# Performance work log

Measured on AMD Instinct MI355X. Metric: run time of the kernel, lower is better.

The kernel has to match this reference:

```python
import jax, jax.numpy as jnp
import numpy as np

B, N, C, H, M, T, L = 2, 4096, 256, 8, 48, 10000, 256
CH = C // H
HID = 512  # mlp_ratio=2


def _ln(x, g, b, eps=1e-5):
    mu = x.mean(-1, keepdims=True)
    var = ((x - mu) ** 2).mean(-1, keepdims=True)
    return (x - mu) * jax.lax.rsqrt(var + eps) * g + b


def setup_inputs() -> dict:
    key = jax.random.key(0)
    ks = iter(jax.random.split(key, 40))
    nrm = lambda shape, s=0.02: jax.random.normal(next(ks), shape, jnp.float32) * s
    return dict(
        feat=jax.random.normal(next(ks), (B, N, C), jnp.float32),
        memory=jax.random.normal(next(ks), (B, L, C), jnp.float32),
        member_idx=jax.random.randint(next(ks), (B, N, M), 0, N),
        cluster_mask=jax.random.randint(next(ks), (B, N, M), 0, 2, jnp.int32),
        pe_idx=jax.random.randint(next(ks), (B, N, M), 0, T),
        global_attn=0,
        pre_table=jax.random.normal(next(ks), (T, 5), jnp.float32),
        Wq=nrm((C, C)), bq=jnp.zeros(C), Wkv=nrm((C, 2 * C)), bkv=jnp.zeros(2 * C),
        blank_k=nrm((C,), 1.0), blank_v=nrm((C,), 1.0),
        Wpe=nrm((5, H)), bpe=jnp.zeros(H),
        Wproj=nrm((C, C)), bproj=jnp.zeros(C),
        g1=jnp.ones(C), be1=jnp.zeros(C), g2=jnp.ones(C), be2=jnp.zeros(C),
        xWq=nrm((C, C)), xbq=jnp.zeros(C), xWk=nrm((C, C)), xbk=jnp.zeros(C),
        xWv=nrm((C, C)), xbv=jnp.zeros(C), xWo=nrm((C, C)), xbo=jnp.zeros(C),
        xg=jnp.ones(C), xbe=jnp.zeros(C),
        W1=nrm((C, HID)), bf1=jnp.zeros(HID), W2=nrm((HID, C)), bf2=jnp.zeros(C),
    )


def _cluster_attn(x, member_idx, cluster_mask, pe_idx, pre_table,
                  Wq, bq, Wkv, bkv, blank_k, blank_v, Wpe, bpe, Wproj, bproj):
    b, n, c = x.shape
    scale = CH ** -0.5
    q = ((x @ Wq + bq) * scale).reshape(b, n, H, CH).transpose(0, 2, 1, 3)  # bhnc
    kv = (x @ Wkv + bkv).reshape(b, n, H, 2, CH)
    k = kv[..., 0, :].transpose(0, 2, 1, 3)  # bhnc
    v = kv[..., 1, :].transpose(0, 2, 1, 3)  # bhnc
    # CLUSTENQK: gather per-token neighborhood keys, dot with q -> b h n m
    gather = jax.vmap(lambda t, idx: t[:, idx, :])  # (h,n,c),(n,m)->(h,n,m,c)
    k_g = gather(k, member_idx)
    attn = jnp.einsum('bhnc,bhnmc->bhnm', q, k_g)
    # positional embedding table lookup
    pe_table = pre_table @ Wpe + bpe                 # T x H
    pos = pe_table[pe_idx].transpose(0, 3, 1, 2)     # b h n m
    attn = attn + pos
    maskf = cluster_mask.astype(attn.dtype)[:, None]  # b 1 n m
    attn = attn + (1.0 - maskf) * -100.0
    blank_attn = jnp.einsum('bhnc,hc->bhn', q, blank_k.reshape(H, CH))[..., None]
    p = jax.nn.softmax(jnp.concatenate([attn, blank_attn], axis=-1), axis=-1)
    pa, pb = p[..., :-1], p[..., -1:]
    # CLUSTENAV: gather values, weighted sum
    v_g = gather(v, member_idx)
    out = jnp.einsum('bhnm,bhnmc->bhnc', pa, v_g)
    out = out + pb * blank_v.reshape(1, H, 1, CH)
    out = out.transpose(0, 2, 1, 3).reshape(b, n, c)
    return out @ Wproj + bproj


def _cross_attn(tgt, memory, xWq, xbq, xWk, xbk, xWv, xbv, xWo, xbo, xg, xbe):
    b, n, c = tgt.shape
    t2 = _ln(tgt, xg, xbe)  # normalize_before=True
    q = (t2 @ xWq + xbq).reshape(b, n, H, CH).transpose(0, 2, 1, 3) * (CH ** -0.5)
    k = (memory @ xWk + xbk).reshape(b, -1, H, CH).transpose(0, 2, 1, 3)
    v = (memory @ xWv + xbv).reshape(b, -1, H, CH).transpose(0, 2, 1, 3)
    p = jax.nn.softmax(jnp.einsum('bhnc,bhlc->bhnl', q, k), axis=-1)
    o = jnp.einsum('bhnl,bhlc->bhnc', p, v).transpose(0, 2, 1, 3).reshape(b, n, c)
    return tgt + (o @ xWo + xbo)


def reference(feat, memory, member_idx, cluster_mask, pe_idx, global_attn, pre_table,
              Wq, bq, Wkv, bkv, blank_k, blank_v, Wpe, bpe, Wproj, bproj,
              g1, be1, g2, be2,
              xWq, xbq, xWk, xbk, xWv, xbv, xWo, xbo, xg, xbe,
              W1, bf1, W2, bf2):
    # global_attn is a static flag; this reference covers the local-cluster path
    assert global_attn == 0
    # local cluster attention with pre-norm residual (drop_path/layer_scale disabled)
    feat = feat + _cluster_attn(_ln(feat, g1, be1), member_idx, cluster_mask, pe_idx,
                                pre_table, Wq, bq, Wkv, bkv, blank_k, blank_v,
                                Wpe, bpe, Wproj, bproj)
    # cross attention to memory (pre-norm, residual inside)
    feat = _cross_attn(feat, memory, xWq, xbq, xWk, xbk, xWv, xbv, xWo, xbo, xg, xbe)
    # MLP block
    h = jax.nn.gelu(_ln(feat, g2, be2) @ W1 + bf1, approximate=False)
    feat = feat + (h @ W2 + bf2)
    return feat
```

## Files before the change

kernel.cpp:

```cpp
#include <hip/hip_runtime.h>
#include <hip/hip_bf16.h>
#include <hip/hip_fp8.h>
#include <math.h>

#define BB 2
#define NN 4096
#define CC 256
#define HH 8
#define MM 48
#define TT 10000
#define LL 256
#define CHDIM 32
#define HIDD 512
#define ROWS (BB*NN)

typedef __attribute__((ext_vector_type(8))) short bf16x8;
typedef __attribute__((ext_vector_type(4))) float f32x4;
typedef __attribute__((ext_vector_type(2))) float f32x2;

static __device__ __forceinline__ short f2bf(float x) {
    __hip_bfloat16 h = __float2bfloat16(x);
    return *reinterpret_cast<short*>(&h);
}
static __device__ __forceinline__ float bf2f(short s) {
    unsigned int u = ((unsigned int)(unsigned short)s) << 16;
    union { unsigned int u; float f; } c; c.u = u;
    return c.f;
}

struct WtDesc { const float* src; __hip_bfloat16* dst; int K; int N; int tile0; float scl; };
struct WtArgs { WtDesc d[9]; };

__global__ __launch_bounds__(256) void prep_all_kernel(WtArgs a,
    const float* __restrict__ pre, const float* __restrict__ Wpe,
    const float* __restrict__ bpe, float* __restrict__ pet,
    const float* __restrict__ bq, const float* __restrict__ bkv,
    const float* __restrict__ xbk, const float* __restrict__ xbv,
    const float* __restrict__ xbq, float scale,
    float* __restrict__ bqkv, float* __restrict__ xbkv, float* __restrict__ xbqS,
    const float* __restrict__ memory, __hip_bfloat16* __restrict__ memBf) {
    __shared__ float tile[32][33];
    int bid = blockIdx.x, tid = threadIdx.x;
    if (bid < 768) {
        int mi = 0;
        #pragma unroll
        for (int i = 1; i < 9; ++i) if (bid >= a.d[i].tile0) mi = i;
        WtDesc dsc = a.d[mi];
        int t = bid - dsc.tile0;
        int tiles_n = dsc.N >> 5;
        int k0 = (t / tiles_n) * 32, n0 = (t % tiles_n) * 32;
        int tx = tid & 31, ty = tid >> 5;
        #pragma unroll
        for (int i = 0; i < 32; i += 8)
            tile[ty + i][tx] = dsc.src[(size_t)(k0 + ty + i) * dsc.N + n0 + tx];
        __syncthreads();
        #pragma unroll
        for (int i = 0; i < 32; i += 8)
            dsc.dst[(size_t)(n0 + ty + i) * dsc.K + k0 + tx] = __float2bfloat16(tile[tx][ty + i] * dsc.scl);
        return;
    }
    bid -= 768;
    if (bid < 313) {
        int i = bid * 256 + tid;
        if (i >= TT * HH) return;
        int t = i / HH, h = i % HH;
        float s = bpe[h];
        #pragma unroll
        for (int j = 0; j < 5; ++j) s += pre[t * 5 + j] * Wpe[j * HH + h];
        pet[i] = s;
    } else if (bid < 319) {
        int i = (bid - 313) * 256 + tid;
        if (i < 256) bqkv[i] = bq[i] * scale;
        else if (i < 768) bqkv[i] = bkv[i - 256];
        else if (i < 1024) xbkv[i - 768] = xbk[i - 768];
        else if (i < 1280) xbkv[256 + i - 1024] = xbv[i - 1024];
        else if (i < 1536) xbqS[i - 1280] = xbq[i - 1280] * scale;
    } else {
        int i = (bid - 319) * 256 + tid;
        if (i < 131072) memBf[i] = __float2bfloat16(memory[i]);
    }
}

__global__ __launch_bounds__(256) void ln_kernel(const float* __restrict__ in,
                                                 const float* __restrict__ g,
                                                 const float* __restrict__ b,
                                                 __hip_bfloat16* __restrict__ out) {
    int wave = threadIdx.x >> 6, lane = threadIdx.x & 63;
    int row = blockIdx.x * 4 + wave;
    float4 v = ((const float4*)(in + (size_t)row * CC))[lane];
    float s = (v.x + v.y) + (v.z + v.w);
    #pragma unroll
    for (int off = 32; off; off >>= 1) s += __shfl_xor(s, off, 64);
    float mu = s * (1.0f / 256.0f);
    float dx = v.x - mu, dy = v.y - mu, dz = v.z - mu, dw = v.w - mu;
    float s2 = (dx * dx + dy * dy) + (dz * dz + dw * dw);
    #pragma unroll
    for (int off = 32; off; off >>= 1) s2 += __shfl_xor(s2, off, 64);
    float rs = rsqrtf(s2 * (1.0f / 256.0f) + 1e-5f);
    float4 g4 = ((const float4*)g)[lane];
    float4 b4 = ((const float4*)b)[lane];
    ushort4 o4;
    o4.x = (unsigned short)f2bf(dx * rs * g4.x + b4.x);
    o4.y = (unsigned short)f2bf(dy * rs * g4.y + b4.y);
    o4.z = (unsigned short)f2bf(dz * rs * g4.z + b4.z);
    o4.w = (unsigned short)f2bf(dw * rs * g4.w + b4.w);
    *(ushort4*)((unsigned short*)out + (size_t)row * CC + lane * 4) = o4;
}

#define GBM 64
#define GBN 64
#define GBK 64
#define LDA 72
template<int ACT, int OUTM>
__device__ __forceinline__ void gemm_body(short* As, short* Bs,
    const __hip_bfloat16* __restrict__ A, const __hip_bfloat16* __restrict__ BT,
    const float* __restrict__ bias, void* __restrict__ outv,
    const float* __restrict__ residual, int N, int K, int row0, int col0,
    void* __restrict__ outv2) {
    int tid = threadIdx.x;
    int lane = tid & 63, wid = tid >> 6;
    int wr = wid >> 1, wc = wid & 1;
    int lr = lane & 15, lk = lane >> 4;
    f32x4 acc[2][2] = {};
    for (int kt = 0; kt < K; kt += GBK) {
        #pragma unroll
        for (int i = 0; i < 2; ++i) {
            int flat = tid + i * 256;
            int r = flat >> 3, kc = (flat & 7) * 8;
            *(bf16x8*)&As[r * LDA + kc] = *(const bf16x8*)(A + (size_t)(row0 + r) * K + kt + kc);
        }
        #pragma unroll
        for (int i = 0; i < 2; ++i) {
            int flat = tid + i * 256;
            int r = flat >> 3, kc = (flat & 7) * 8;
            *(bf16x8*)&Bs[r * LDA + kc] = *(const bf16x8*)(BT + (size_t)(col0 + r) * K + kt + kc);
        }
        __syncthreads();
        #pragma unroll
        for (int ks = 0; ks < 2; ++ks) {
            bf16x8 bfr[2];
            #pragma unroll
            for (int n = 0; n < 2; ++n)
                bfr[n] = *(const bf16x8*)&Bs[(wc * 32 + n * 16 + lr) * LDA + ks * 32 + lk * 8];
            #pragma unroll
            for (int m = 0; m < 2; ++m) {
                bf16x8 afr = *(const bf16x8*)&As[(wr * 32 + m * 16 + lr) * LDA + ks * 32 + lk * 8];
                #pragma unroll
                for (int n = 0; n < 2; ++n)
                    acc[m][n] = __builtin_amdgcn_mfma_f32_16x16x32_bf16(afr, bfr[n], acc[m][n], 0, 0, 0);
            }
        }
        __syncthreads();
    }
    float bv[2];
    #pragma unroll
    for (int n = 0; n < 2; ++n) bv[n] = bias[col0 + wc * 32 + n * 16 + lr];
    #pragma unroll
    for (int m = 0; m < 2; ++m) {
        #pragma unroll
        for (int n = 0; n < 2; ++n) {
            int col = col0 + wc * 32 + n * 16 + lr;
            #pragma unroll
            for (int r = 0; r < 4; ++r) {
                int row = row0 + wr * 32 + m * 16 + lk * 4 + r;
                float v = acc[m][n][r] + bv[n];
                if (ACT == 1) {
                    float z = v + 0.044715f * v * v * v;
                    v = v / (1.0f + __expf(-1.5957691216057308f * z));
                }
                if (OUTM == 2) {
                    if (col < 256) {
                        ((__hip_bfloat16*)outv)[(size_t)row * 256 + col] = __float2bfloat16(v);
                    } else {
                        __hip_fp8_e4m3 f8(v);
                        ((unsigned char*)outv2)[(size_t)row * 512 + (col - 256)] = f8.__x;
                    }
                } else {
                    size_t oi = (size_t)row * N + col;
                    if (residual) v += residual[oi];
                    if (OUTM == 1) ((__hip_bfloat16*)outv)[oi] = __float2bfloat16(v);
                    else ((float*)outv)[oi] = v;
                }
            }
        }
    }
}

template<int ACT, int OUTM>
__global__ __launch_bounds__(256) void mfma_gemm_kernel(
    const __hip_bfloat16* __restrict__ A, const __hip_bfloat16* __restrict__ BT,
    const float* __restrict__ bias, void* __restrict__ outv,
    const float* __restrict__ residual, int M, int N, int K,
    void* __restrict__ outv2) {
    __shared__ short As[GBM * LDA];
    __shared__ short Bs[GBN * LDA];
    gemm_body<ACT, OUTM>(As, Bs, A, BT, bias, outv, residual, N, K,
                         blockIdx.y * GBM, blockIdx.x * GBN, outv2);
}

struct GemmPair {
    const __hip_bfloat16 *A1, *B1; const float* bias1; void* out1;
    const __hip_bfloat16 *A2, *B2; const float* bias2; void* out2;
};
__global__ __launch_bounds__(256) void dual_gemm_kernel(GemmPair p) {
    __shared__ short As[GBM * LDA];
    __shared__ short Bs[GBN * LDA];
    if (blockIdx.x < 4) {
        gemm_body<0, 1>(As, Bs, p.A1, p.B1, p.bias1, p.out1, nullptr, 256, 256,
                        blockIdx.y * GBM, blockIdx.x * GBN, nullptr);
    } else {
        int row0 = blockIdx.y * GBM;
        if (row0 >= 512) return;
        gemm_body<0, 1>(As, Bs, p.A2, p.B2, p.bias2, p.out2, nullptr, 512, 256,
                        row0, (blockIdx.x - 4) * GBN, nullptr);
    }
}

#define KVSTR8 528
__global__ __launch_bounds__(512) void cluster_attn_kernel(
    const __hip_bfloat16* __restrict__ qh,
    const unsigned char* __restrict__ kv8,
    const int* __restrict__ member_idx, const int* __restrict__ cluster_mask,
    const int* __restrict__ pe_idx, const float* __restrict__ pet,
    const float* __restrict__ blank_k, const float* __restrict__ blank_v,
    __hip_bfloat16* __restrict__ outp) {
    const short* qg = (const short*)qh;
    __shared__ unsigned char s_kv[48 * KVSTR8];
    __shared__ float s_pm[48 * 9];
    __shared__ float s_q[256];
    int tid = threadIdx.x;
    int bid = blockIdx.x;
    int row = ((bid & 7) << 10) | (bid >> 3);
    int b = row >> 12;

    {
        int w = tid >> 6, l = tid & 63;
        #pragma unroll
        for (int r = 0; r < 6; ++r) {
            int m = w + r * 8;
            int im = member_idx[(size_t)row * MM + m];
            uint2 v8 = *(const uint2*)(kv8 + ((size_t)(b * NN + im)) * 512 + l * 8);
            *(uint2*)&s_kv[m * KVSTR8 + l * 8] = v8;
        }
    }
    if (tid < MM) {
        float mb = cluster_mask[(size_t)row * MM + tid] ? 0.0f : -100.0f;
        int pidx = pe_idx[(size_t)row * MM + tid];
        const float4* pr = (const float4*)(pet + (size_t)pidx * 8);
        float4 p0 = pr[0], p1 = pr[1];
        float* dst = &s_pm[tid * 9];
        dst[0] = p0.x + mb; dst[1] = p0.y + mb; dst[2] = p0.z + mb; dst[3] = p0.w + mb;
        dst[4] = p1.x + mb; dst[5] = p1.y + mb; dst[6] = p1.z + mb; dst[7] = p1.w + mb;
    } else if (tid >= 256) {
        s_q[tid - 256] = bf2f(qg[(size_t)row * CC + (tid - 256)]);
    }
    __syncthreads();

    int h = tid >> 6, lane = tid & 63;
    const float* qf = s_q + h * CHDIM;
    float e = 0.0f;
    if (lane < MM) {
        const uint4* kp = (const uint4*)(s_kv + lane * KVSTR8 + h * 64);
        uint4 kw0 = kp[0];
        uint4 kw1 = kp[1];
        unsigned int kws[8] = {kw0.x, kw0.y, kw0.z, kw0.w, kw1.x, kw1.y, kw1.z, kw1.w};
        float d0 = s_pm[lane * 9 + h], d1 = 0.0f;
        #pragma unroll
        for (int u = 0; u < 8; u += 2) {
            f32x2 a01 = __builtin_amdgcn_cvt_pk_f32_fp8(kws[u], 0);
            f32x2 a23 = __builtin_amdgcn_cvt_pk_f32_fp8(kws[u], 1);
            f32x2 b01 = __builtin_amdgcn_cvt_pk_f32_fp8(kws[u + 1], 0);
            f32x2 b23 = __builtin_amdgcn_cvt_pk_f32_fp8(kws[u + 1], 1);
            d0 += qf[u * 4 + 0] * a01.x + qf[u * 4 + 1] * a01.y
                + qf[u * 4 + 2] * a23.x + qf[u * 4 + 3] * a23.y;
            d1 += qf[u * 4 + 4] * b01.x + qf[u * 4 + 5] * b01.y
                + qf[u * 4 + 6] * b23.x + qf[u * 4 + 7] * b23.y;
        }
        e = __expf(d0 + d1);
    } else if (lane == MM) {
        const float* bk = blank_k + h * CHDIM;
        float d = 0.0f;
        #pragma unroll
        for (int c = 0; c < CHDIM; ++c) d += qf[c] * bk[c];
        e = __expf(d);
    }
    float ssum = e;
    #pragma unroll
    for (int off = 32; off; off >>= 1) ssum += __shfl_xor(ssum, off, 64);
    float p = e / ssum;
    float p48 = __shfl(p, MM, 64);

    int mg = lane >> 3, cq = lane & 7;
    unsigned int vw[6];
    #pragma unroll
    for (int it = 0; it < 6; ++it)
        vw[it] = *(const unsigned int*)(s_kv + (it * 8 + mg) * KVSTR8 + h * 64 + 32 + cq * 4);
    float a0 = 0.f, a1 = 0.f, a2 = 0.f, a3 = 0.f;
    #pragma unroll
    for (int it = 0; it < 6; ++it) {
        int m = it * 8 + mg;
        float pm = __shfl(p, m, 64);
        f32x2 v01 = __builtin_amdgcn_cvt_pk_f32_fp8(vw[it], 0);
        f32x2 v23 = __builtin_amdgcn_cvt_pk_f32_fp8(vw[it], 1);
        a0 += pm * v01.x; a1 += pm * v01.y;
        a2 += pm * v23.x; a3 += pm * v23.y;
    }
    #pragma unroll
    for (int off = 8; off < 64; off <<= 1) {
        a0 += __shfl_xor(a0, off, 64);
        a1 += __shfl_xor(a1, off, 64);
        a2 += __shfl_xor(a2, off, 64);
        a3 += __shfl_xor(a3, off, 64);
    }
    if (lane < 8) {
        const float* bvp = blank_v + h * CHDIM + cq * 4;
        a0 += p48 * bvp[0]; a1 += p48 * bvp[1]; a2 += p48 * bvp[2]; a3 += p48 * bvp[3];
        ushort4 o4;
        o4.x = (unsigned short)f2bf(a0); o4.y = (unsigned short)f2bf(a1);
        o4.z = (unsigned short)f2bf(a2); o4.w = (unsigned short)f2bf(a3);
        *(ushort4*)((unsigned short*)outp + (size_t)row * CC + h * CHDIM + cq * 4) = o4;
    }
}

#define KSLD 40
#define PVLD 264
__global__ __launch_bounds__(256) void cross_attn_kernel(
    const __hip_bfloat16* __restrict__ xq,
    const __hip_bfloat16* __restrict__ xkvh,
    __hip_bfloat16* __restrict__ o) {
    const short* xkv = (const short*)xkvh;
    extern __shared__ short lds[];
    short* Ks = lds;
    short* Vt = lds + 256 * KSLD;
    short* Ps = Vt + 32 * PVLD;
    int tid = threadIdx.x, lane = tid & 63, w = tid >> 6;
    int tile = blockIdx.x, h = blockIdx.y, b = blockIdx.z;
    int lr = lane & 15, g = lane >> 4;

    #pragma unroll
    for (int p = 0; p < 8; ++p) {
        int l = p * 32 + (tid >> 3);
        int c4 = (tid & 7) * 4;
        const short* kvrow = xkv + ((size_t)(b * LL + l)) * 512 + h * CHDIM;
        ushort4 kk = *(const ushort4*)(kvrow + c4);
        *(ushort4*)&Ks[l * KSLD + c4] = kk;
        ushort4 vv = *(const ushort4*)(kvrow + 256 + c4);
        Vt[(c4 + 0) * PVLD + l] = vv.x;
        Vt[(c4 + 1) * PVLD + l] = vv.y;
        Vt[(c4 + 2) * PVLD + l] = vv.z;
        Vt[(c4 + 3) * PVLD + l] = vv.w;
    }
    __syncthreads();

    int qrow = b * NN + tile * 64 + w * 16 + lr;
    bf16x8 afr = *(const bf16x8*)(xq + (size_t)qrow * CC + h * CHDIM + g * 8);
    f32x4 s[16];
    #pragma unroll
    for (int t = 0; t < 16; ++t) {
        bf16x8 kb = *(const bf16x8*)&Ks[(t * 16 + lr) * KSLD + g * 8];
        s[t] = __builtin_amdgcn_mfma_f32_16x16x32_bf16(afr, kb, (f32x4){0.f,0.f,0.f,0.f}, 0, 0, 0);
    }
    float rs[4] = {0.f, 0.f, 0.f, 0.f};
    #pragma unroll
    for (int t = 0; t < 16; ++t)
        #pragma unroll
        for (int r = 0; r < 4; ++r) { float e = __expf(s[t][r]); s[t][r] = e; rs[r] += e; }
    #pragma unroll
    for (int off = 1; off < 16; off <<= 1)
        #pragma unroll
        for (int r = 0; r < 4; ++r) rs[r] += __shfl_xor(rs[r], off, 64);
    short* Pw = Ps + w * 16 * PVLD;
    #pragma unroll
    for (int t = 0; t < 16; ++t)
        #pragma unroll
        for (int r = 0; r < 4; ++r)
            Pw[(g * 4 + r) * PVLD + t * 16 + lr] = f2bf(s[t][r]);
    f32x4 oacc[2] = {};
    #pragma unroll
    for (int kc = 0; kc < 8; ++kc) {
        bf16x8 pa = *(const bf16x8*)&Pw[lr * PVLD + kc * 32 + g * 8];
        #pragma unroll
        for (int n = 0; n < 2; ++n) {
            bf16x8 vb = *(const bf16x8*)&Vt[(n * 16 + lr) * PVLD + kc * 32 + g * 8];
            oacc[n] = __builtin_amdgcn_mfma_f32_16x16x32_bf16(pa, vb, oacc[n], 0, 0, 0);
        }
    }
    float inv[4];
    #pragma unroll
    for (int r = 0; r < 4; ++r) inv[r] = 1.0f / rs[r];
    #pragma unroll
    for (int n = 0; n < 2; ++n)
        #pragma unroll
        for (int r = 0; r < 4; ++r) {
            int orow = b * NN + tile * 64 + w * 16 + g * 4 + r;
            o[(size_t)orow * CC + h * CHDIM + n * 16 + lr] = __float2bfloat16(oacc[n][r] * inv[r]);
        }
}

extern "C" void kernel_launch(void* const* d_in, const int* in_sizes, int n_in,
                              void* d_out, int out_size, void* d_ws, size_t ws_size,
                              hipStream_t stream) {
    const float* feat        = (const float*)d_in[0];
    const float* memory      = (const float*)d_in[1];
    const int*   member_idx  = (const int*)d_in[2];
    const int*   cluster_mask= (const int*)d_in[3];
    const int*   pe_idx      = (const int*)d_in[4];
    const float* pre_table   = (const float*)d_in[6];
    const float* Wq    = (const float*)d_in[7];
    const float* bq    = (const float*)d_in[8];
    const float* Wkv   = (const float*)d_in[9];
    const float* bkv   = (const float*)d_in[10];
    const float* blank_k = (const float*)d_in[11];
    const float* blank_v = (const float*)d_in[12];
    const float* Wpe   = (const float*)d_in[13];
    const float* bpe   = (const float*)d_in[14];
    const float* Wproj = (const float*)d_in[15];
    const float* bproj = (const float*)d_in[16];
    const float* g1    = (const float*)d_in[17];
    const float* be1   = (const float*)d_in[18];
    const float* g2    = (const float*)d_in[19];
    const float* be2   = (const float*)d_in[20];
    const float* xWq   = (const float*)d_in[21];
    const float* xbq   = (const float*)d_in[22];
    const float* xWk   = (const float*)d_in[23];
    const float* xbk   = (const float*)d_in[24];
    const float* xWv   = (const float*)d_in[25];
    const float* xbv   = (const float*)d_in[26];
    const float* xWo   = (const float*)d_in[27];
    const float* xbo   = (const float*)d_in[28];
    const float* xg    = (const float*)d_in[29];
    const float* xbe   = (const float*)d_in[30];
    const float* W1    = (const float*)d_in[31];
    const float* bf1   = (const float*)d_in[32];
    const float* W2    = (const float*)d_in[33];
    const float* bf2   = (const float*)d_in[34];
    float* out = (float*)d_out;
    float* ws  = (float*)d_ws;

    __hip_bfloat16* qBf   = (__hip_bfloat16*)ws;
    __hip_bfloat16* xqBf  = (__hip_bfloat16*)ws;
    unsigned char*  kv8   = (unsigned char*)(ws + 1048576);
    __hip_bfloat16* xkvBf = (__hip_bfloat16*)(ws + 2097152);
    __hip_bfloat16* hBf   = (__hip_bfloat16*)(ws + 2228224);
    float* feat1F = ws + 4325376;
    __hip_bfloat16* aBf   = (__hip_bfloat16*)(ws + 6422528);
    __hip_bfloat16* oBf   = (__hip_bfloat16*)(ws + 7471104);
    __hip_bfloat16* WqkvT = (__hip_bfloat16*)(ws + 8519680);
    __hip_bfloat16* WprojT= (__hip_bfloat16*)(ws + 8617984);
    __hip_bfloat16* xWqT  = (__hip_bfloat16*)(ws + 8650752);
    __hip_bfloat16* xWoT  = (__hip_bfloat16*)(ws + 8683520);
    __hip_bfloat16* xWkvT = (__hip_bfloat16*)(ws + 8716288);
    __hip_bfloat16* W1T   = (__hip_bfloat16*)(ws + 8781824);
    __hip_bfloat16* W2T   = (__hip_bfloat16*)(ws + 8847360);
    __hip_bfloat16* memBf = (__hip_bfloat16*)(ws + 8912896);
    float* pet   = ws + 8978432;
    float* bqkv  = ws + 9058432;
    float* xbkv  = ws + 9059200;
    float* xbqS  = ws + 9059712;

    const float scale = 0.17677669529663689f;

    WtArgs wa;
    wa.d[0] = { Wq,    WqkvT,          256, 256, 0,   scale };
    wa.d[1] = { Wkv,   WqkvT + 65536,  256, 512, 64,  1.0f };
    wa.d[2] = { Wproj, WprojT,         256, 256, 192, 1.0f };
    wa.d[3] = { xWq,   xWqT,           256, 256, 256, scale };
    wa.d[4] = { xWk,   xWkvT,          256, 256, 320, 1.0f };
    wa.d[5] = { xWv,   xWkvT + 65536,  256, 256, 384, 1.0f };
    wa.d[6] = { xWo,   xWoT,           256, 256, 448, 1.0f };
    wa.d[7] = { W1,    W1T,            256, 512, 512, 1.0f };
    wa.d[8] = { W2,    W2T,            512, 256, 640, 1.0f };
    prep_all_kernel<<<768 + 831, 256, 0, stream>>>(wa, pre_table, Wpe, bpe, pet,
                                                   bq, bkv, xbk, xbv, xbq, scale,
                                                   bqkv, xbkv, xbqS, memory, memBf);

    ln_kernel<<<ROWS / 4, 256, 0, stream>>>(feat, g1, be1, aBf);
    mfma_gemm_kernel<0,2><<<dim3(12, 128), 256, 0, stream>>>(aBf, WqkvT, bqkv, qBf, nullptr, ROWS, 768, 256, kv8);
    cluster_attn_kernel<<<ROWS, 512, 0, stream>>>(qBf, kv8, member_idx, cluster_mask, pe_idx, pet, blank_k, blank_v, oBf);
    mfma_gemm_kernel<0,0><<<dim3(4, 128), 256, 0, stream>>>(oBf, WprojT, bproj, feat1F, feat, ROWS, 256, 256, nullptr);
    ln_kernel<<<ROWS / 4, 256, 0, stream>>>(feat1F, xg, xbe, aBf);
    {
        GemmPair gp;
        gp.A1 = aBf;   gp.B1 = xWqT;  gp.bias1 = xbqS; gp.out1 = xqBf;
        gp.A2 = memBf; gp.B2 = xWkvT; gp.bias2 = xbkv; gp.out2 = xkvBf;
        dual_gemm_kernel<<<dim3(12, 128), 256, 0, stream>>>(gp);
    }
    {
        size_t xlds = (256 * KSLD + 32 * PVLD + 4 * 16 * PVLD) * sizeof(short);
        cross_attn_kernel<<<dim3(NN / 64, HH, BB), 256, xlds, stream>>>(xqBf, xkvBf, oBf);
    }
    mfma_gemm_kernel<0,0><<<dim3(4, 128), 256, 0, stream>>>(oBf, xWoT, xbo, out, feat1F, ROWS, 256, 256, nullptr);
    ln_kernel<<<ROWS / 4, 256, 0, stream>>>(out, g2, be2, aBf);
    mfma_gemm_kernel<1,1><<<dim3(8, 128), 256, 0, stream>>>(aBf, W1T, bf1, hBf, nullptr, ROWS, HIDD, 256, nullptr);
    mfma_gemm_kernel<0,0><<<dim3(4, 128), 256, 0, stream>>>(hBf, W2T, bf2, out, out, ROWS, 256, HIDD, nullptr);
}
```

Measured before the change: 148.8 us.

## Process two rows per cluster-attention block with prefetched second-row gather

Each cluster attention block now handles two consecutive rows. The second row's KV gather and q load are issued into registers before the first row's compute runs, so they overlap with it, and are then staged into a second LDS buffer. The PE/mask bias is now read directly per lane from global memory instead of being staged in LDS, and the LDS row stride is reduced. This halves the block count and hides gather latency, at the cost of extra registers, an extra barrier and less parallelism per block.

```diff
diff --git a/kernel.cpp b/kernel.cpp
--- a/kernel.cpp
+++ b/kernel.cpp
@@ -216,7 +216,78 @@
     }
 }
 
-#define KVSTR8 528
+#define KVSTR8 520
+__device__ __forceinline__ void cluster_compute_row(
+    const unsigned char* s_kvr, const float* s_qr, int row, int b, int w, int lane,
+    const int* __restrict__ cluster_mask, const int* __restrict__ pe_idx,
+    const float* __restrict__ pet, const float* __restrict__ blank_k,
+    const float* __restrict__ blank_v, __hip_bfloat16* __restrict__ outp) {
+    int h = w;
+    const float* qf = s_qr + h * CHDIM;
+    float e = 0.0f;
+    if (lane < MM) {
+        const unsigned int* kp = (const unsigned int*)(s_kvr + lane * KVSTR8 + h * 64);
+        float d0 = pet[(size_t)pe_idx[(size_t)row * MM + lane] * HH + h];
+        if (cluster_mask[(size_t)row * MM + lane] == 0) d0 -= 100.0f;
+        float d1 = 0.0f;
+        #pragma unroll
+        for (int u = 0; u < 8; u += 2) {
+            unsigned int ka = kp[u], kb = kp[u + 1];
+            f32x2 a01 = __builtin_amdgcn_cvt_pk_f32_fp8(ka, 0);
+            f32x2 a23 = __builtin_amdgcn_cvt_pk_f32_fp8(ka, 1);
+            f32x2 b01 = __builtin_amdgcn_cvt_pk_f32_fp8(kb, 0);
+            f32x2 b23 = __builtin_amdgcn_cvt_pk_f32_fp8(kb, 1);
+            d0 += qf[u * 4 + 0] * a01.x + qf[u * 4 + 1] * a01.y
+                + qf[u * 4 + 2] * a23.x + qf[u * 4 + 3] * a23.y;
+            d1 += qf[u * 4 + 4] * b01.x + qf[u * 4 + 5] * b01.y
+                + qf[u * 4 + 6] * b23.x + qf[u * 4 + 7] * b23.y;
+        }
+        e = __expf(d0 + d1);
+    } else if (lane == MM) {
+        const float* bk = blank_k + h * CHDIM;
+        float d = 0.0f;
+        #pragma unroll
+        for (int c = 0; c < CHDIM; ++c) d += qf[c] * bk[c];
+        e = __expf(d);
+    }
+    float ssum = e;
+    #pragma unroll
+    for (int off = 32; off; off >>= 1) ssum += __shfl_xor(ssum, off, 64);
+    float p = e / ssum;
+    float p48 = __shfl(p, MM, 64);
+
+    int mg = lane >> 3, cq = lane & 7;
+    unsigned int vw[6];
+    #pragma unroll
+    for (int it = 0; it < 6; ++it)
+        vw[it] = *(const unsigned int*)(s_kvr + (it * 8 + mg) * KVSTR8 + h * 64 + 32 + cq * 4);
+    float a0 = 0.f, a1 = 0.f, a2 = 0.f, a3 = 0.f;
+    #pragma unroll
+    for (int it = 0; it < 6; ++it) {
+        int m = it * 8 + mg;
+        float pm = __shfl(p, m, 64);
+        f32x2 v01 = __builtin_amdgcn_cvt_pk_f32_fp8(vw[it], 0);
+        f32x2 v23 = __builtin_amdgcn_cvt_pk_f32_fp8(vw[it], 1);
+        a0 += pm * v01.x; a1 += pm * v01.y;
+        a2 += pm * v23.x; a3 += pm * v23.y;
+    }
+    #pragma unroll
+    for (int off = 8; off < 64; off <<= 1) {
+        a0 += __shfl_xor(a0, off, 64);
+        a1 += __shfl_xor(a1, off, 64);
+        a2 += __shfl_xor(a2, off, 64);
+        a3 += __shfl_xor(a3, off, 64);
+    }
+    if (lane < 8) {
+        const float* bvp = blank_v + h * CHDIM + cq * 4;
+        a0 += p48 * bvp[0]; a1 += p48 * bvp[1]; a2 += p48 * bvp[2]; a3 += p48 * bvp[3];
+        ushort4 o4;
+        o4.x = (unsigned short)f2bf(a0); o4.y = (unsigned short)f2bf(a1);
+        o4.z = (unsigned short)f2bf(a2); o4.w = (unsigned short)f2bf(a3);
+        *(ushort4*)((unsigned short*)outp + (size_t)row * CC + h * CHDIM + cq * 4) = o4;
+    }
+}
+
 __global__ __launch_bounds__(512) void cluster_attn_kernel(
     const __hip_bfloat16* __restrict__ qh,
     const unsigned char* __restrict__ kv8,
@@ -225,101 +296,46 @@
     const float* __restrict__ blank_k, const float* __restrict__ blank_v,
     __hip_bfloat16* __restrict__ outp) {
     const short* qg = (const short*)qh;
-    __shared__ unsigned char s_kv[48 * KVSTR8];
-    __shared__ float s_pm[48 * 9];
-    __shared__ float s_q[256];
+    __shared__ unsigned char s_kv[2][48 * KVSTR8];
+    __shared__ float s_q[2][256];
     int tid = threadIdx.x;
     int bid = blockIdx.x;
-    int row = ((bid & 7) << 10) | (bid >> 3);
-    int b = row >> 12;
-
-    {
-        int w = tid >> 6, l = tid & 63;
-        #pragma unroll
-        for (int r = 0; r < 6; ++r) {
-            int m = w + r * 8;
-            int im = member_idx[(size_t)row * MM + m];
-            uint2 v8 = *(const uint2*)(kv8 + ((size_t)(b * NN + im)) * 512 + l * 8);
-            *(uint2*)&s_kv[m * KVSTR8 + l * 8] = v8;
-        }
-    }
-    if (tid < MM) {
-        float mb = cluster_mask[(size_t)row * MM + tid] ? 0.0f : -100.0f;
-        int pidx = pe_idx[(size_t)row * MM + tid];
-        const float4* pr = (const float4*)(pet + (size_t)pidx * 8);
-        float4 p0 = pr[0], p1 = pr[1];
-        float* dst = &s_pm[tid * 9];
-        dst[0] = p0.x + mb; dst[1] = p0.y + mb; dst[2] = p0.z + mb; dst[3] = p0.w + mb;
-        dst[4] = p1.x + mb; dst[5] = p1.y + mb; dst[6] = p1.z + mb; dst[7] = p1.w + mb;
-    } else if (tid >= 256) {
-        s_q[tid - 256] = bf2f(qg[(size_t)row * CC + (tid - 256)]);
-    }
+    int pairIdx = ((bid & 7) << 9) | (bid >> 3);
+    int row0 = pairIdx * 2;
+    int row1 = row0 + 1;
+    int b = row0 >> 12;
+    int w = tid >> 6, l = tid & 63;
+
+    int im1[6];
+    #pragma unroll
+    for (int r = 0; r < 6; ++r) {
+        int m = w + r * 8;
+        im1[r] = member_idx[(size_t)row1 * MM + m];
+        int im0 = member_idx[(size_t)row0 * MM + m];
+        uint2 v8 = *(const uint2*)(kv8 + ((size_t)(b * NN + im0)) * 512 + l * 8);
+        *(uint2*)&s_kv[0][m * KVSTR8 + l * 8] = v8;
+    }
+    if (tid >= 256) s_q[0][tid - 256] = bf2f(qg[(size_t)row0 * CC + (tid - 256)]);
     __syncthreads();
 
-    int h = tid >> 6, lane = tid & 63;
-    const float* qf = s_q + h * CHDIM;
-    float e = 0.0f;
-    if (lane < MM) {
-        const uint4* kp = (const uint4*)(s_kv + lane * KVSTR8 + h * 64);
-        uint4 kw0 = kp[0];
-        uint4 kw1 = kp[1];
-        unsigned int kws[8] = {kw0.x, kw0.y, kw0.z, kw0.w, kw1.x, kw1.y, kw1.z, kw1.w};
-        float d0 = s_pm[lane * 9 + h], d1 = 0.0f;
-        #pragma unroll
-        for (int u = 0; u < 8; u += 2) {
-            f32x2 a01 = __builtin_amdgcn_cvt_pk_f32_fp8(kws[u], 0);
-            f32x2 a23 = __builtin_amdgcn_cvt_pk_f32_fp8(kws[u], 1);
-            f32x2 b01 = __builtin_amdgcn_cvt_pk_f32_fp8(kws[u + 1], 0);
-            f32x2 b23 = __builtin_amdgcn_cvt_pk_f32_fp8(kws[u + 1], 1);
-            d0 += qf[u * 4 + 0] * a01.x + qf[u * 4 + 1] * a01.y
-                + qf[u * 4 + 2] * a23.x + qf[u * 4 + 3] * a23.y;
-            d1 += qf[u * 4 + 4] * b01.x + qf[u * 4 + 5] * b01.y
-                + qf[u * 4 + 6] * b23.x + qf[u * 4 + 7] * b23.y;
-        }
-        e = __expf(d0 + d1);
-    } else if (lane == MM) {
-        const float* bk = blank_k + h * CHDIM;
-        float d = 0.0f;
-        #pragma unroll
-        for (int c = 0; c < CHDIM; ++c) d += qf[c] * bk[c];
-        e = __expf(d);
-    }
-    float ssum = e;
-    #pragma unroll
-    for (int off = 32; off; off >>= 1) ssum += __shfl_xor(ssum, off, 64);
-    float p = e / ssum;
-    float p48 = __shfl(p, MM, 64);
-
-    int mg = lane >> 3, cq = lane & 7;
-    unsigned int vw[6];
-    #pragma unroll
-    for (int it = 0; it < 6; ++it)
-        vw[it] = *(const unsigned int*)(s_kv + (it * 8 + mg) * KVSTR8 + h * 64 + 32 + cq * 4);
-    float a0 = 0.f, a1 = 0.f, a2 = 0.f, a3 = 0.f;
-    #pragma unroll
-    for (int it = 0; it < 6; ++it) {
-        int m = it * 8 + mg;
-        float pm = __shfl(p, m, 64);
-        f32x2 v01 = __builtin_amdgcn_cvt_pk_f32_fp8(vw[it], 0);
-        f32x2 v23 = __builtin_amdgcn_cvt_pk_f32_fp8(vw[it], 1);
-        a0 += pm * v01.x; a1 += pm * v01.y;
-        a2 += pm * v23.x; a3 += pm * v23.y;
-    }
-    #pragma unroll
-    for (int off = 8; off < 64; off <<= 1) {
-        a0 += __shfl_xor(a0, off, 64);
-        a1 += __shfl_xor(a1, off, 64);
-        a2 += __shfl_xor(a2, off, 64);
-        a3 += __shfl_xor(a3, off, 64);
-    }
-    if (lane < 8) {
-        const float* bvp = blank_v + h * CHDIM + cq * 4;
-        a0 += p48 * bvp[0]; a1 += p48 * bvp[1]; a2 += p48 * bvp[2]; a3 += p48 * bvp[3];
-        ushort4 o4;
-        o4.x = (unsigned short)f2bf(a0); o4.y = (unsigned short)f2bf(a1);
-        o4.z = (unsigned short)f2bf(a2); o4.w = (unsigned short)f2bf(a3);
-        *(ushort4*)((unsigned short*)outp + (size_t)row * CC + h * CHDIM + cq * 4) = o4;
-    }
+    uint2 kvreg[6];
+    #pragma unroll
+    for (int r = 0; r < 6; ++r)
+        kvreg[r] = *(const uint2*)(kv8 + ((size_t)(b * NN + im1[r])) * 512 + l * 8);
+    float q1reg = 0.0f;
+    if (tid >= 256) q1reg = bf2f(qg[(size_t)row1 * CC + (tid - 256)]);
+
+    cluster_compute_row(s_kv[0], s_q[0], row0, b, w, l,
+                        cluster_mask, pe_idx, pet, blank_k, blank_v, outp);
+
+    #pragma unroll
+    for (int r = 0; r < 6; ++r)
+        *(uint2*)&s_kv[1][(w + r * 8) * KVSTR8 + l * 8] = kvreg[r];
+    if (tid >= 256) s_q[1][tid - 256] = q1reg;
+    __syncthreads();
+
+    cluster_compute_row(s_kv[1], s_q[1], row1, b, w, l,
+                        cluster_mask, pe_idx, pet, blank_k, blank_v, outp);
 }
 
 #define KSLD 40
@@ -476,7 +492,7 @@
 
     ln_kernel<<<ROWS / 4, 256, 0, stream>>>(feat, g1, be1, aBf);
     mfma_gemm_kernel<0,2><<<dim3(12, 128), 256, 0, stream>>>(aBf, WqkvT, bqkv, qBf, nullptr, ROWS, 768, 256, kv8);
-    cluster_attn_kernel<<<ROWS, 512, 0, stream>>>(qBf, kv8, member_idx, cluster_mask, pe_idx, pet, blank_k, blank_v, oBf);
+    cluster_attn_kernel<<<ROWS / 2, 512, 0, stream>>>(qBf, kv8, member_idx, cluster_mask, pe_idx, pet, blank_k, blank_v, oBf);
     mfma_gemm_kernel<0,0><<<dim3(4, 128), 256, 0, stream>>>(oBf, WprojT, bproj, feat1F, feat, ROWS, 256, 256, nullptr);
     ln_kernel<<<ROWS / 4, 256, 0, stream>>>(feat1F, xg, xbe, aBf);
     {
```

After: 165.7 us. 11.4% more time.
